# Kernel optimization log

Hardware: AMD Instinct MI355X
Metric: run time of the kernel (lower is better)

Reference implementation:

```python
import jax, jax.numpy as jnp
import numpy as np

B, C, H, W = 4, 64, 256, 256
HEADS = 8
WIN = 8            # window_size = (8, 8)
SPA_INNER = 64


def setup_inputs() -> dict:
    key = jax.random.key(0)
    ks = jax.random.split(key, 13)
    r = lambda k, s: jax.random.normal(k, s, dtype=jnp.float32)
    lin = lambda k, out_d, in_d: r(k, (out_d, in_d)) * (1.0 / np.sqrt(in_d))
    seq = WIN * WIN
    return {
        "x": r(ks[0], (B, C, H, W)),
        "pan_feature": r(ks[1], (B, C // 2, H, W)),
        "W_pan_q": lin(ks[2], SPA_INNER // 2, C // 2),
        "W_pan_k": lin(ks[3], SPA_INNER // 2, C // 2),
        "W_v1": lin(ks[4], SPA_INNER, C),
        "W_v2": lin(ks[5], SPA_INNER, C),
        "W_k2": lin(ks[6], SPA_INNER // 2, C),
        "W_q1c": lin(ks[7], SPA_INNER // 2, C),
        "W_k1c": lin(ks[8], SPA_INNER // 2, C),
        "W_inner_out": lin(ks[9], C, SPA_INNER),
        "W_inter_out": lin(ks[10], C, SPA_INNER),
        # trunc_normal_(std=1, a=-2, b=2) learned positional biases
        "pos_inner": jnp.clip(r(ks[11], (1, HEADS, seq, seq)), -2.0, 2.0),
        "pos_color": jnp.clip(r(ks[12], (1, HEADS, SPA_INNER // 2, SPA_INNER // 2)), -2.0, 2.0),
    }


def _mha(q, k, v, pos, heads, scale):
    # q,k,v: [B', n, h*d]  -> standard MHA with additive positional bias
    Bp, n, _ = q.shape
    sp = lambda t: t.reshape(Bp, n, heads, -1).transpose(0, 2, 1, 3)  # b h n d
    qh, kh, vh = sp(q) * scale, sp(k), sp(v)
    attn = jax.nn.softmax(jnp.einsum('bhid,bhjd->bhij', qh, kh) + pos, axis=-1)
    o = jnp.einsum('bhij,bhjd->bhid', attn, vh)
    return o.transpose(0, 2, 1, 3).reshape(Bp, n, -1)


def _mha_color(q, k, v, pos, heads, scale):
    # torch rearranges 'b (h d) n -> b h n d': dim1 (window area) is split
    # into heads, attention runs over the channel axis (dim2).
    Bp, hd, n = q.shape
    sp = lambda t: t.reshape(Bp, heads, hd // heads, n).transpose(0, 1, 3, 2)  # b h n d
    qh, kh, vh = sp(q) * scale, sp(k), sp(v)
    attn = jax.nn.softmax(jnp.einsum('bhid,bhjd->bhij', qh, kh) + pos, axis=-1)
    o = jnp.einsum('bhij,bhjd->bhid', attn, vh)
    return o.transpose(0, 1, 3, 2).reshape(Bp, hd, n)


def _inter_attn(q, k, v, heads):
    # elementwise cosine-similarity gating over the head-dim, no softmax
    Bp, n, dq = q.shape
    qh = q.reshape(Bp, n, heads, dq // heads).transpose(0, 2, 3, 1)  # b h d n
    kh = k.reshape(Bp, n, heads, dq // heads).transpose(0, 2, 3, 1)
    vh = v.reshape(Bp, n, heads, -1).transpose(0, 2, 1, 3)           # b h n d
    cos = jnp.sum(qh * kh, axis=2) / (jnp.linalg.norm(qh, axis=2) * jnp.linalg.norm(kh, axis=2))  # b h n
    o = cos[..., None] * vh
    return o.transpose(0, 2, 1, 3).reshape(Bp, n, -1)


def reference(x, pan_feature, W_pan_q, W_pan_k, W_v1, W_v2, W_k2, W_q1c, W_k1c,
              W_inner_out, W_inter_out, pos_inner, pos_color):
    b, c, h, w = x.shape
    hl = wl = WIN
    hn, wn = h // hl, w // wl

    def part(t):  # b c (hn hl) (wn wl) -> (b hn wn) (hl wl) c
        bb, cc = t.shape[0], t.shape[1]
        return t.reshape(bb, cc, hn, hl, wn, wl).transpose(0, 2, 4, 3, 5, 1).reshape(bb * hn * wn, hl * wl, cc)

    pan = part(pan_feature)       # [B', 64, c//2]
    xf = part(x)                  # [B', 64, c]

    pan_q = pan @ W_pan_q.T       # [B', 64, spa_inner//2]
    pan_k = pan @ W_pan_k.T
    x_v1 = xf @ W_v1.T            # [B', 64, spa_inner]
    half = x_v1.shape[-1] // 2
    v1_pan, v1_color = x_v1[..., :half], x_v1[..., half:]

    # inner spatial attention (scale uses inner_dim=spa_inner_dim, as in source)
    scale_inner = (SPA_INNER // HEADS) ** -0.5
    out_pan = _mha(pan_q, pan_k, v1_pan, pos_inner, HEADS, scale_inner)

    # inner color attention (scale uses inner_dim=window area)
    q1c = xf @ W_q1c.T
    k1c = xf @ W_k1c.T
    scale_color = ((hl * wl) // HEADS) ** -0.5
    out_color = _mha_color(q1c, k1c, v1_color, pos_color, HEADS, scale_color)

    out = jnp.concatenate([out_pan, out_color], axis=-1) @ W_inner_out.T  # [B', 64, c]
    x_v2 = out @ W_v2.T
    x_k2 = out @ W_k2.T
    out = _inter_attn(pan_q, x_k2, x_v2, HEADS)
    out = out @ W_inter_out.T     # [B', 64, c]

    cc = out.shape[-1]
    # (b hn wn) (hl wl) c -> b c (hn hl) (wn wl)
    out = out.reshape(b, hn, wn, hl, wl, cc).transpose(0, 5, 1, 3, 2, 4).reshape(b, cc, h, w)
    return out
```

## Files before the change

kernel.cpp:

```cpp
#include <hip/hip_runtime.h>


typedef __attribute__((ext_vector_type(8))) short short8;
typedef __attribute__((ext_vector_type(4))) float floatx4;

#define CCH  64
#define HH   256
#define WWD  256
#define HWsz (HH*WWD)
#define CHW  (CCH*HH*WWD)

#define OWPQ  0
#define OWPK  1024
#define OWV1  2048
#define OWV2  6144
#define OWK2  10240
#define OWQ1C 12288
#define OWK1C 14336
#define OWIO  16384
#define OWINT 20480
#define WTOT  24576

__device__ __forceinline__ unsigned int f2bf_u(float f) {
    unsigned int u = __builtin_bit_cast(unsigned int, f);
    u += 0x7FFFu + ((u >> 16) & 1u);
    return u >> 16;
}
__device__ __forceinline__ float bfu2f(unsigned int b) {
    return __builtin_bit_cast(float, b << 16);
}

template <int K, int N, int SA, int SO>
__device__ __forceinline__ void proj(const float* __restrict__ A,
                                     const unsigned short* __restrict__ Wh,
                                     const unsigned short* __restrict__ Wl,
                                     float* __restrict__ O,
                                     int wave, int lane) {
    constexpr int KS = K / 32;
    constexpr int NT = N / 16;
    const int l15 = lane & 15;
    const int quad = lane >> 4;
    const int m0 = wave * 16;

    union Frag { short8 v; unsigned int u[4]; };
    Frag ah[KS], al[KS];
#pragma unroll
    for (int kk = 0; kk < KS; ++kk) {
        const float4* ap = (const float4*)(A + (m0 + l15) * SA + kk * 32 + quad * 8);
        float4 fa = ap[0], fb = ap[1];
        float ff[8] = {fa.x, fa.y, fa.z, fa.w, fb.x, fb.y, fb.z, fb.w};
#pragma unroll
        for (int j2 = 0; j2 < 4; ++j2) {
            float f0 = ff[2 * j2], f1 = ff[2 * j2 + 1];
            unsigned int h0 = f2bf_u(f0), h1 = f2bf_u(f1);
            float r0 = f0 - bfu2f(h0), r1 = f1 - bfu2f(h1);
            ah[kk].u[j2] = h0 | (h1 << 16);
            al[kk].u[j2] = f2bf_u(r0) | (f2bf_u(r1) << 16);
        }
    }

#pragma unroll
    for (int nt = 0; nt < NT; ++nt) {
        floatx4 acc = {0.f, 0.f, 0.f, 0.f};
#pragma unroll
        for (int kk = 0; kk < KS; ++kk) {
            const int wo = (nt * 16 + l15) * K + kk * 32 + quad * 8;
            short8 bh = *(const short8*)(Wh + wo);
            short8 bl = *(const short8*)(Wl + wo);
            acc = __builtin_amdgcn_mfma_f32_16x16x32_bf16(ah[kk].v, bh, acc, 0, 0, 0);
            acc = __builtin_amdgcn_mfma_f32_16x16x32_bf16(al[kk].v, bh, acc, 0, 0, 0);
            acc = __builtin_amdgcn_mfma_f32_16x16x32_bf16(ah[kk].v, bl, acc, 0, 0, 0);
        }
#pragma unroll
        for (int r = 0; r < 4; ++r)
            O[(m0 + quad * 4 + r) * SO + nt * 16 + l15] = acc[r];
    }
}

__global__ void cvt_w(const float* __restrict__ w0, const float* __restrict__ w1,
                      const float* __restrict__ w2, const float* __restrict__ w3,
                      const float* __restrict__ w4, const float* __restrict__ w5,
                      const float* __restrict__ w6, const float* __restrict__ w7,
                      const float* __restrict__ w8, unsigned short* __restrict__ o) {
    int i = blockIdx.x * 256 + threadIdx.x;
    const float* src; int off;
    if      (i < 1024)  { src = w0; off = 0; }
    else if (i < 2048)  { src = w1; off = 1024; }
    else if (i < 6144)  { src = w2; off = 2048; }
    else if (i < 10240) { src = w3; off = 6144; }
    else if (i < 12288) { src = w4; off = 10240; }
    else if (i < 14336) { src = w5; off = 12288; }
    else if (i < 16384) { src = w6; off = 14336; }
    else if (i < 20480) { src = w7; off = 16384; }
    else                { src = w8; off = 20480; }
    float f = src[i - off];
    unsigned int h = f2bf_u(f);
    o[i] = (unsigned short)h;
    o[WTOT + i] = (unsigned short)f2bf_u(f - bfu2f(h));
}

__global__ __launch_bounds__(256, 2) void in2ma_main(
    const float* __restrict__ x, const float* __restrict__ pan,
    const float* __restrict__ posi, const float* __restrict__ posc,
    const unsigned short* __restrict__ wb, float* __restrict__ out) {
    __shared__ __align__(16) float s_xf[64 * 68];
    __shared__ __align__(16) float s_cat[64 * 68];
    __shared__ __align__(16) float s_v1[64 * 66];
    __shared__ __align__(16) float s_qk[64 * 66];
    __shared__ __align__(16) float s_k2[64 * 34];

    const int tid  = threadIdx.x;
    const int wave = tid >> 6;
    const int lane = tid & 63;
    const int wid  = blockIdx.x;
    const int b    = wid >> 10;
    const int hn_i = (wid >> 5) & 31;
    const int wn_i = wid & 31;
    const int h0 = hn_i * 8, w0 = wn_i * 8;

    const float scale = 0.35355339059327373f;
    const unsigned short* wlo = wb + WTOT;

    {
        const int c = tid >> 2, i = tid & 3;
        const float* xp = x + (size_t)b * CHW + (size_t)c * HWsz + (size_t)h0 * WWD + w0;
#pragma unroll
        for (int r = 0; r < 2; ++r) {
            const int hl = i * 2 + r;
            const float4* p = (const float4*)(xp + hl * WWD);
            float4 a = p[0], q = p[1];
            float* d = s_xf + (hl * 8) * 68 + c;
            d[0 * 68] = a.x; d[1 * 68] = a.y; d[2 * 68] = a.z; d[3 * 68] = a.w;
            d[4 * 68] = q.x; d[5 * 68] = q.y; d[6 * 68] = q.z; d[7 * 68] = q.w;
        }
        if (tid < 128) {
            const int c2 = tid >> 2, i2 = tid & 3;
            const float* pp = pan + (size_t)b * (CHW / 2) + (size_t)c2 * HWsz + (size_t)h0 * WWD + w0;
#pragma unroll
            for (int r = 0; r < 2; ++r) {
                const int hl = i2 * 2 + r;
                const float4* p = (const float4*)(pp + hl * WWD);
                float4 a = p[0], q = p[1];
                float* d = s_cat + (hl * 8) * 68 + c2;
                d[0 * 68] = a.x; d[1 * 68] = a.y; d[2 * 68] = a.z; d[3 * 68] = a.w;
                d[4 * 68] = q.x; d[5 * 68] = q.y; d[6 * 68] = q.z; d[7 * 68] = q.w;
            }
        }
    }
    __syncthreads();

    proj<32, 32, 68, 66>(s_cat,      wb + OWPQ,  wlo + OWPQ,  s_qk,      wave, lane);
    proj<32, 32, 68, 66>(s_cat,      wb + OWPK,  wlo + OWPK,  s_qk + 32, wave, lane);
    proj<64, 64, 68, 66>(s_xf,       wb + OWV1,  wlo + OWV1,  s_v1,      wave, lane);
    proj<64, 32, 68, 68>(s_xf,       wb + OWQ1C, wlo + OWQ1C, s_cat + 32, wave, lane);
    proj<64, 32, 68, 34>(s_xf,       wb + OWK1C, wlo + OWK1C, s_k2,      wave, lane);
    __syncthreads();

#pragma unroll
    for (int hh = 0; hh < 2; ++hh) {
        const int h = wave + hh * 4;
        const float* qp = s_qk + lane * 66 + 4 * h;
        float q0 = qp[0], q1 = qp[1], q2 = qp[2], q3 = qp[3];
        const float4* pp4 = (const float4*)(posi + h * 4096 + lane * 64);
        float lrow[64];
        float s = 0.f;
#pragma unroll
        for (int t4 = 0; t4 < 16; ++t4) {
            float4 pv = pp4[t4];
            float pvv[4] = {pv.x, pv.y, pv.z, pv.w};
#pragma unroll
            for (int u = 0; u < 4; ++u) {
                const int t = t4 * 4 + u;
                const float* kp = s_qk + t * 66 + 32 + 4 * h;
                float d = q0 * kp[0] + q1 * kp[1] + q2 * kp[2] + q3 * kp[3];
                float e = __expf(d * scale + pvv[u]);
                lrow[t] = e; s += e;
            }
        }
        const float inv = 1.f / s;
        float o0 = 0.f, o1 = 0.f, o2 = 0.f, o3 = 0.f;
#pragma unroll
        for (int t = 0; t < 64; ++t) {
            const float* vp = s_v1 + t * 66 + 4 * h;
            float p = lrow[t];
            o0 += p * vp[0]; o1 += p * vp[1]; o2 += p * vp[2]; o3 += p * vp[3];
        }
        float* op = s_cat + lane * 68 + 4 * h;
        op[0] = o0 * inv; op[1] = o1 * inv; op[2] = o2 * inv; op[3] = o3 * inv;
    }

    {
        const int h = wave * 2 + (lane >> 5);
        const int i = lane & 31;
        float q[8];
#pragma unroll
        for (int j = 0; j < 8; ++j) q[j] = s_cat[(8 * h + j) * 68 + 32 + i];
        float lr[32];
#pragma unroll
        for (int j = 0; j < 8; ++j) {
            const float* kp = s_k2 + (8 * h + j) * 34;
            const float qj = q[j];
#pragma unroll
            for (int t = 0; t < 32; ++t) {
                float kv = kp[t];
                if (j == 0) lr[t] = qj * kv; else lr[t] += qj * kv;
            }
        }
        const float4* pp4 = (const float4*)(posc + h * 1024 + i * 32);
        float s = 0.f;
#pragma unroll
        for (int t4 = 0; t4 < 8; ++t4) {
            float4 pv = pp4[t4];
            float pvv[4] = {pv.x, pv.y, pv.z, pv.w};
#pragma unroll
            for (int u = 0; u < 4; ++u) {
                const int t = t4 * 4 + u;
                float e = __expf(lr[t] * scale + pvv[u]);
                lr[t] = e; s += e;
            }
        }
        const float inv = 1.f / s;
#pragma unroll
        for (int j = 0; j < 8; ++j) {
            const float* vp = s_v1 + (8 * h + j) * 66 + 32;
            float acc = 0.f;
#pragma unroll
            for (int t = 0; t < 32; ++t) acc += lr[t] * vp[t];
            s_cat[(8 * h + j) * 68 + 32 + i] = acc * inv;
        }
    }
    __syncthreads();

    proj<64, 64, 68, 68>(s_cat, wb + OWIO, wlo + OWIO, s_xf, wave, lane);
    proj<64, 64, 68, 66>(s_xf,  wb + OWV2, wlo + OWV2, s_v1, wave, lane);
    proj<64, 32, 68, 34>(s_xf,  wb + OWK2, wlo + OWK2, s_k2, wave, lane);
    __syncthreads();

    {
        const int t = tid & 63;
        const int hb = tid >> 6;
#pragma unroll
        for (int r = 0; r < 2; ++r) {
            const int h = hb + r * 4;
            const float* qp = s_qk + t * 66 + 4 * h;
            const float* kp = s_k2 + t * 34 + 4 * h;
            float q0 = qp[0], q1 = qp[1], q2 = qp[2], q3 = qp[3];
            float k0 = kp[0], k1 = kp[1], k2 = kp[2], k3 = kp[3];
            float qq = q0 * q0 + q1 * q1 + q2 * q2 + q3 * q3;
            float kk = k0 * k0 + k1 * k1 + k2 * k2 + k3 * k3;
            float qk = q0 * k0 + q1 * k1 + q2 * k2 + q3 * k3;
            float cosv = qk * rsqrtf(qq * kk);
            const float* vp = s_v1 + t * 66 + 8 * h;
            float* op = s_cat + t * 68 + 8 * h;
#pragma unroll
            for (int j = 0; j < 8; ++j) op[j] = cosv * vp[j];
        }
    }
    __syncthreads();

    proj<64, 64, 68, 66>(s_cat, wb + OWINT, wlo + OWINT, s_v1, wave, lane);
    __syncthreads();

    {
        const int c = tid >> 2, i = tid & 3;
        float* op = out + (size_t)b * CHW + (size_t)c * HWsz + (size_t)h0 * WWD + w0;
#pragma unroll
        for (int r = 0; r < 2; ++r) {
            const int hl = i * 2 + r;
            float v[8];
#pragma unroll
            for (int wl = 0; wl < 8; ++wl)
                v[wl] = s_v1[(hl * 8 + wl) * 66 + c];
            float4* q = (float4*)(op + hl * WWD);
            float4 q0; q0.x = v[0]; q0.y = v[1]; q0.z = v[2]; q0.w = v[3];
            float4 q1; q1.x = v[4]; q1.y = v[5]; q1.z = v[6]; q1.w = v[7];
            q[0] = q0; q[1] = q1;
        }
    }
}

extern "C" void kernel_launch(void* const* d_in, const int* in_sizes, int n_in,
                              void* d_out, int out_size, void* d_ws, size_t ws_size,
                              hipStream_t stream) {
    (void)in_sizes; (void)n_in; (void)out_size; (void)ws_size;
    const float* x    = (const float*)d_in[0];
    const float* pan  = (const float*)d_in[1];
    const float* posi = (const float*)d_in[11];
    const float* posc = (const float*)d_in[12];
    unsigned short* wb = (unsigned short*)d_ws;

    cvt_w<<<WTOT / 256, 256, 0, stream>>>(
        (const float*)d_in[2], (const float*)d_in[3], (const float*)d_in[4],
        (const float*)d_in[5], (const float*)d_in[6], (const float*)d_in[7],
        (const float*)d_in[8], (const float*)d_in[9], (const float*)d_in[10], wb);

    in2ma_main<<<4096, 256, 0, stream>>>(x, pan, posi, posc, wb, (float*)d_out);
}
```

Measured before the change: 465.9 us.

## Use 512-thread blocks and split projections across eight waves

Doubles the workgroup to eight waves and redistributes the projection GEMMs and attention heads so each wave handles one head or one slice of a projection. Converted A fragments are reused across projections that read the same input, which cuts repeated fp32-to-split-bf16 conversion. Shared-memory row strides are padded to multiples of four so LDS accesses can use float4. The occupancy target is raised, which adds register pressure, and the inner-output projection is computed redundantly by paired waves.

```diff
diff --git a/kernel.cpp b/kernel.cpp
--- a/kernel.cpp
+++ b/kernel.cpp
@@ -30,22 +30,17 @@
     return __builtin_bit_cast(float, b << 16);
 }
 
-template <int K, int N, int SA, int SO>
-__device__ __forceinline__ void proj(const float* __restrict__ A,
-                                     const unsigned short* __restrict__ Wh,
-                                     const unsigned short* __restrict__ Wl,
-                                     float* __restrict__ O,
-                                     int wave, int lane) {
-    constexpr int KS = K / 32;
-    constexpr int NT = N / 16;
+union Frag { short8 v; unsigned int u[4]; };
+template <int KS> struct AF { Frag ah[KS], al[KS]; };
+
+template <int K, int SA>
+__device__ __forceinline__ AF<K / 32> load_afrag(const float* __restrict__ A,
+                                                 int m0, int lane) {
+    AF<K / 32> f;
     const int l15 = lane & 15;
     const int quad = lane >> 4;
-    const int m0 = wave * 16;
-
-    union Frag { short8 v; unsigned int u[4]; };
-    Frag ah[KS], al[KS];
-#pragma unroll
-    for (int kk = 0; kk < KS; ++kk) {
+#pragma unroll
+    for (int kk = 0; kk < K / 32; ++kk) {
         const float4* ap = (const float4*)(A + (m0 + l15) * SA + kk * 32 + quad * 8);
         float4 fa = ap[0], fb = ap[1];
         float ff[8] = {fa.x, fa.y, fa.z, fa.w, fb.x, fb.y, fb.z, fb.w};
@@ -54,26 +49,36 @@
             float f0 = ff[2 * j2], f1 = ff[2 * j2 + 1];
             unsigned int h0 = f2bf_u(f0), h1 = f2bf_u(f1);
             float r0 = f0 - bfu2f(h0), r1 = f1 - bfu2f(h1);
-            ah[kk].u[j2] = h0 | (h1 << 16);
-            al[kk].u[j2] = f2bf_u(r0) | (f2bf_u(r1) << 16);
-        }
-    }
-
+            f.ah[kk].u[j2] = h0 | (h1 << 16);
+            f.al[kk].u[j2] = f2bf_u(r0) | (f2bf_u(r1) << 16);
+        }
+    }
+    return f;
+}
+
+template <int K, int SO, int NT>
+__device__ __forceinline__ void mm(const AF<K / 32>& f,
+                                   const unsigned short* __restrict__ Wh,
+                                   const unsigned short* __restrict__ Wl,
+                                   float* __restrict__ O,
+                                   int m0, int n0, int lane) {
+    const int l15 = lane & 15;
+    const int quad = lane >> 4;
 #pragma unroll
     for (int nt = 0; nt < NT; ++nt) {
         floatx4 acc = {0.f, 0.f, 0.f, 0.f};
 #pragma unroll
-        for (int kk = 0; kk < KS; ++kk) {
-            const int wo = (nt * 16 + l15) * K + kk * 32 + quad * 8;
+        for (int kk = 0; kk < K / 32; ++kk) {
+            const int wo = (n0 + nt * 16 + l15) * K + kk * 32 + quad * 8;
             short8 bh = *(const short8*)(Wh + wo);
             short8 bl = *(const short8*)(Wl + wo);
-            acc = __builtin_amdgcn_mfma_f32_16x16x32_bf16(ah[kk].v, bh, acc, 0, 0, 0);
-            acc = __builtin_amdgcn_mfma_f32_16x16x32_bf16(al[kk].v, bh, acc, 0, 0, 0);
-            acc = __builtin_amdgcn_mfma_f32_16x16x32_bf16(ah[kk].v, bl, acc, 0, 0, 0);
+            acc = __builtin_amdgcn_mfma_f32_16x16x32_bf16(f.ah[kk].v, bh, acc, 0, 0, 0);
+            acc = __builtin_amdgcn_mfma_f32_16x16x32_bf16(f.al[kk].v, bh, acc, 0, 0, 0);
+            acc = __builtin_amdgcn_mfma_f32_16x16x32_bf16(f.ah[kk].v, bl, acc, 0, 0, 0);
         }
 #pragma unroll
         for (int r = 0; r < 4; ++r)
-            O[(m0 + quad * 4 + r) * SO + nt * 16 + l15] = acc[r];
+            O[(m0 + quad * 4 + r) * SO + n0 + nt * 16 + l15] = acc[r];
     }
 }
 
@@ -99,15 +104,15 @@
     o[WTOT + i] = (unsigned short)f2bf_u(f - bfu2f(h));
 }
 
-__global__ __launch_bounds__(256, 2) void in2ma_main(
+__global__ __launch_bounds__(512, 4) void in2ma_main(
     const float* __restrict__ x, const float* __restrict__ pan,
     const float* __restrict__ posi, const float* __restrict__ posc,
     const unsigned short* __restrict__ wb, float* __restrict__ out) {
     __shared__ __align__(16) float s_xf[64 * 68];
     __shared__ __align__(16) float s_cat[64 * 68];
-    __shared__ __align__(16) float s_v1[64 * 66];
-    __shared__ __align__(16) float s_qk[64 * 66];
-    __shared__ __align__(16) float s_k2[64 * 34];
+    __shared__ __align__(16) float s_v1[64 * 68];
+    __shared__ __align__(16) float s_qk[64 * 68];
+    __shared__ __align__(16) float s_k2[64 * 36];
 
     const int tid  = threadIdx.x;
     const int wave = tid >> 6;
@@ -122,48 +127,50 @@
     const unsigned short* wlo = wb + WTOT;
 
     {
-        const int c = tid >> 2, i = tid & 3;
-        const float* xp = x + (size_t)b * CHW + (size_t)c * HWsz + (size_t)h0 * WWD + w0;
-#pragma unroll
-        for (int r = 0; r < 2; ++r) {
-            const int hl = i * 2 + r;
-            const float4* p = (const float4*)(xp + hl * WWD);
-            float4 a = p[0], q = p[1];
-            float* d = s_xf + (hl * 8) * 68 + c;
-            d[0 * 68] = a.x; d[1 * 68] = a.y; d[2 * 68] = a.z; d[3 * 68] = a.w;
-            d[4 * 68] = q.x; d[5 * 68] = q.y; d[6 * 68] = q.z; d[7 * 68] = q.w;
-        }
-        if (tid < 128) {
-            const int c2 = tid >> 2, i2 = tid & 3;
-            const float* pp = pan + (size_t)b * (CHW / 2) + (size_t)c2 * HWsz + (size_t)h0 * WWD + w0;
-#pragma unroll
-            for (int r = 0; r < 2; ++r) {
-                const int hl = i2 * 2 + r;
-                const float4* p = (const float4*)(pp + hl * WWD);
-                float4 a = p[0], q = p[1];
-                float* d = s_cat + (hl * 8) * 68 + c2;
-                d[0 * 68] = a.x; d[1 * 68] = a.y; d[2 * 68] = a.z; d[3 * 68] = a.w;
-                d[4 * 68] = q.x; d[5 * 68] = q.y; d[6 * 68] = q.z; d[7 * 68] = q.w;
-            }
-        }
-    }
-    __syncthreads();
-
-    proj<32, 32, 68, 66>(s_cat,      wb + OWPQ,  wlo + OWPQ,  s_qk,      wave, lane);
-    proj<32, 32, 68, 66>(s_cat,      wb + OWPK,  wlo + OWPK,  s_qk + 32, wave, lane);
-    proj<64, 64, 68, 66>(s_xf,       wb + OWV1,  wlo + OWV1,  s_v1,      wave, lane);
-    proj<64, 32, 68, 68>(s_xf,       wb + OWQ1C, wlo + OWQ1C, s_cat + 32, wave, lane);
-    proj<64, 32, 68, 34>(s_xf,       wb + OWK1C, wlo + OWK1C, s_k2,      wave, lane);
-    __syncthreads();
-
-#pragma unroll
-    for (int hh = 0; hh < 2; ++hh) {
-        const int h = wave + hh * 4;
-        const float* qp = s_qk + lane * 66 + 4 * h;
-        float q0 = qp[0], q1 = qp[1], q2 = qp[2], q3 = qp[3];
+        const int c = lane, hl = wave;
+        const float* xp = x + (size_t)b * CHW + (size_t)c * HWsz
+                            + (size_t)(h0 + hl) * WWD + w0;
+        const float4* p = (const float4*)xp;
+        float4 a = p[0], q = p[1];
+        float* d = s_xf + (hl * 8) * 68 + c;
+        d[0 * 68] = a.x; d[1 * 68] = a.y; d[2 * 68] = a.z; d[3 * 68] = a.w;
+        d[4 * 68] = q.x; d[5 * 68] = q.y; d[6 * 68] = q.z; d[7 * 68] = q.w;
+        if (wave < 4) {
+            const int hl2 = wave * 2 + (lane >> 5);
+            const int c2 = lane & 31;
+            const float* pp = pan + (size_t)b * (CHW / 2) + (size_t)c2 * HWsz
+                                  + (size_t)(h0 + hl2) * WWD + w0;
+            const float4* p2 = (const float4*)pp;
+            float4 a2 = p2[0], q2 = p2[1];
+            float* d2 = s_cat + (hl2 * 8) * 68 + c2;
+            d2[0 * 68] = a2.x; d2[1 * 68] = a2.y; d2[2 * 68] = a2.z; d2[3 * 68] = a2.w;
+            d2[4 * 68] = q2.x; d2[5 * 68] = q2.y; d2[6 * 68] = q2.z; d2[7 * 68] = q2.w;
+        }
+    }
+    __syncthreads();
+
+    if (wave < 4) {
+        AF<2> f = load_afrag<64, 68>(s_xf, wave * 16, lane);
+        mm<64, 68, 4>(f, wb + OWV1, wlo + OWV1, s_v1, wave * 16, 0, lane);
+        AF<1> g = load_afrag<32, 68>(s_cat, wave * 16, lane);
+        mm<32, 68, 2>(g, wb + OWPQ, wlo + OWPQ, s_qk, wave * 16, 0, lane);
+    } else {
+        const int s = wave - 4;
+        AF<2> f = load_afrag<64, 68>(s_xf, s * 16, lane);
+        mm<64, 68, 2>(f, wb + OWQ1C, wlo + OWQ1C, s_cat + 32, s * 16, 0, lane);
+        mm<64, 36, 2>(f, wb + OWK1C, wlo + OWK1C, s_k2, s * 16, 0, lane);
+        AF<1> g = load_afrag<32, 68>(s_cat, s * 16, lane);
+        mm<32, 68, 2>(g, wb + OWPK, wlo + OWPK, s_qk + 32, s * 16, 0, lane);
+    }
+    __syncthreads();
+
+    {
+        const int h = wave;
+        const float4 qv = *(const float4*)(s_qk + lane * 68 + 4 * h);
+        const float q0 = qv.x, q1 = qv.y, q2 = qv.z, q3 = qv.w;
         const float4* pp4 = (const float4*)(posi + h * 4096 + lane * 64);
         float lrow[64];
-        float s = 0.f;
+        float sden = 0.f;
 #pragma unroll
         for (int t4 = 0; t4 < 16; ++t4) {
             float4 pv = pp4[t4];
@@ -171,25 +178,25 @@
 #pragma unroll
             for (int u = 0; u < 4; ++u) {
                 const int t = t4 * 4 + u;
-                const float* kp = s_qk + t * 66 + 32 + 4 * h;
-                float d = q0 * kp[0] + q1 * kp[1] + q2 * kp[2] + q3 * kp[3];
+                const float4 kv = *(const float4*)(s_qk + t * 68 + 32 + 4 * h);
+                float d = q0 * kv.x + q1 * kv.y + q2 * kv.z + q3 * kv.w;
                 float e = __expf(d * scale + pvv[u]);
-                lrow[t] = e; s += e;
+                lrow[t] = e; sden += e;
             }
         }
-        const float inv = 1.f / s;
+        const float inv = 1.f / sden;
         float o0 = 0.f, o1 = 0.f, o2 = 0.f, o3 = 0.f;
 #pragma unroll
         for (int t = 0; t < 64; ++t) {
-            const float* vp = s_v1 + t * 66 + 4 * h;
+            const float4 vv = *(const float4*)(s_v1 + t * 68 + 4 * h);
             float p = lrow[t];
-            o0 += p * vp[0]; o1 += p * vp[1]; o2 += p * vp[2]; o3 += p * vp[3];
-        }
-        float* op = s_cat + lane * 68 + 4 * h;
-        op[0] = o0 * inv; op[1] = o1 * inv; op[2] = o2 * inv; op[3] = o3 * inv;
-    }
-
-    {
+            o0 += p * vv.x; o1 += p * vv.y; o2 += p * vv.z; o3 += p * vv.w;
+        }
+        float4 ov; ov.x = o0 * inv; ov.y = o1 * inv; ov.z = o2 * inv; ov.w = o3 * inv;
+        *(float4*)(s_cat + lane * 68 + 4 * h) = ov;
+    }
+
+    if (wave < 4) {
         const int h = wave * 2 + (lane >> 5);
         const int i = lane & 31;
         float q[8];
@@ -198,7 +205,7 @@
         float lr[32];
 #pragma unroll
         for (int j = 0; j < 8; ++j) {
-            const float* kp = s_k2 + (8 * h + j) * 34;
+            const float* kp = s_k2 + (8 * h + j) * 36;
             const float qj = q[j];
 #pragma unroll
             for (int t = 0; t < 32; ++t) {
@@ -207,7 +214,7 @@
             }
         }
         const float4* pp4 = (const float4*)(posc + h * 1024 + i * 32);
-        float s = 0.f;
+        float sden = 0.f;
 #pragma unroll
         for (int t4 = 0; t4 < 8; ++t4) {
             float4 pv = pp4[t4];
@@ -216,13 +223,13 @@
             for (int u = 0; u < 4; ++u) {
                 const int t = t4 * 4 + u;
                 float e = __expf(lr[t] * scale + pvv[u]);
-                lr[t] = e; s += e;
+                lr[t] = e; sden += e;
             }
         }
-        const float inv = 1.f / s;
+        const float inv = 1.f / sden;
 #pragma unroll
         for (int j = 0; j < 8; ++j) {
-            const float* vp = s_v1 + (8 * h + j) * 66 + 32;
+            const float* vp = s_v1 + (8 * h + j) * 68 + 32;
             float acc = 0.f;
 #pragma unroll
             for (int t = 0; t < 32; ++t) acc += lr[t] * vp[t];
@@ -231,51 +238,55 @@
     }
     __syncthreads();
 
-    proj<64, 64, 68, 68>(s_cat, wb + OWIO, wlo + OWIO, s_xf, wave, lane);
-    proj<64, 64, 68, 66>(s_xf,  wb + OWV2, wlo + OWV2, s_v1, wave, lane);
-    proj<64, 32, 68, 34>(s_xf,  wb + OWK2, wlo + OWK2, s_k2, wave, lane);
-    __syncthreads();
-
-    {
-        const int t = tid & 63;
-        const int hb = tid >> 6;
-#pragma unroll
-        for (int r = 0; r < 2; ++r) {
-            const int h = hb + r * 4;
-            const float* qp = s_qk + t * 66 + 4 * h;
-            const float* kp = s_k2 + t * 34 + 4 * h;
-            float q0 = qp[0], q1 = qp[1], q2 = qp[2], q3 = qp[3];
-            float k0 = kp[0], k1 = kp[1], k2 = kp[2], k3 = kp[3];
-            float qq = q0 * q0 + q1 * q1 + q2 * q2 + q3 * q3;
-            float kk = k0 * k0 + k1 * k1 + k2 * k2 + k3 * k3;
-            float qk = q0 * k0 + q1 * k1 + q2 * k2 + q3 * k3;
-            float cosv = qk * rsqrtf(qq * kk);
-            const float* vp = s_v1 + t * 66 + 8 * h;
-            float* op = s_cat + t * 68 + 8 * h;
-#pragma unroll
-            for (int j = 0; j < 8; ++j) op[j] = cosv * vp[j];
-        }
-    }
-    __syncthreads();
-
-    proj<64, 64, 68, 66>(s_cat, wb + OWINT, wlo + OWINT, s_v1, wave, lane);
-    __syncthreads();
-
-    {
-        const int c = tid >> 2, i = tid & 3;
-        float* op = out + (size_t)b * CHW + (size_t)c * HWsz + (size_t)h0 * WWD + w0;
-#pragma unroll
-        for (int r = 0; r < 2; ++r) {
-            const int hl = i * 2 + r;
-            float v[8];
-#pragma unroll
-            for (int wl = 0; wl < 8; ++wl)
-                v[wl] = s_v1[(hl * 8 + wl) * 66 + c];
-            float4* q = (float4*)(op + hl * WWD);
-            float4 q0; q0.x = v[0]; q0.y = v[1]; q0.z = v[2]; q0.w = v[3];
-            float4 q1; q1.x = v[4]; q1.y = v[5]; q1.z = v[6]; q1.w = v[7];
-            q[0] = q0; q[1] = q1;
-        }
+    {
+        const int s = wave & 3;
+        AF<2> f = load_afrag<64, 68>(s_cat, s * 16, lane);
+        mm<64, 68, 4>(f, wb + OWIO, wlo + OWIO, s_xf, s * 16, 0, lane);
+        AF<2> g = load_afrag<64, 68>(s_xf, s * 16, lane);
+        if (wave < 4)
+            mm<64, 68, 4>(g, wb + OWV2, wlo + OWV2, s_v1, s * 16, 0, lane);
+        else
+            mm<64, 36, 2>(g, wb + OWK2, wlo + OWK2, s_k2, s * 16, 0, lane);
+    }
+    __syncthreads();
+
+    {
+        const int t = lane, h = wave;
+        const float4 qv = *(const float4*)(s_qk + t * 68 + 4 * h);
+        const float4 kv = *(const float4*)(s_k2 + t * 36 + 4 * h);
+        float qq = qv.x * qv.x + qv.y * qv.y + qv.z * qv.z + qv.w * qv.w;
+        float kk = kv.x * kv.x + kv.y * kv.y + kv.z * kv.z + kv.w * kv.w;
+        float qk = qv.x * kv.x + qv.y * kv.y + qv.z * kv.z + qv.w * kv.w;
+        float cosv = qk * rsqrtf(qq * kk);
+        const float4* vp = (const float4*)(s_v1 + t * 68 + 8 * h);
+        float4* op = (float4*)(s_cat + t * 68 + 8 * h);
+        float4 v0 = vp[0], v1 = vp[1];
+        float4 r0, r1;
+        r0.x = cosv * v0.x; r0.y = cosv * v0.y; r0.z = cosv * v0.z; r0.w = cosv * v0.w;
+        r1.x = cosv * v1.x; r1.y = cosv * v1.y; r1.z = cosv * v1.z; r1.w = cosv * v1.w;
+        op[0] = r0; op[1] = r1;
+    }
+    __syncthreads();
+
+    {
+        AF<2> f = load_afrag<64, 68>(s_cat, (wave >> 1) * 16, lane);
+        mm<64, 68, 2>(f, wb + OWINT, wlo + OWINT, s_v1,
+                      (wave >> 1) * 16, (wave & 1) * 32, lane);
+    }
+    __syncthreads();
+
+    {
+        const int c = lane, hl = wave;
+        float* op = out + (size_t)b * CHW + (size_t)c * HWsz
+                        + (size_t)(h0 + hl) * WWD + w0;
+        float v[8];
+#pragma unroll
+        for (int wl = 0; wl < 8; ++wl)
+            v[wl] = s_v1[(hl * 8 + wl) * 68 + c];
+        float4 q0; q0.x = v[0]; q0.y = v[1]; q0.z = v[2]; q0.w = v[3];
+        float4 q1; q1.x = v[4]; q1.y = v[5]; q1.z = v[6]; q1.w = v[7];
+        float4* q = (float4*)op;
+        q[0] = q0; q[1] = q1;
     }
 }
 
@@ -294,5 +305,5 @@
         (const float*)d_in[5], (const float*)d_in[6], (const float*)d_in[7],
         (const float*)d_in[8], (const float*)d_in[9], (const float*)d_in[10], wb);
 
-    in2ma_main<<<4096, 256, 0, stream>>>(x, pan, posi, posc, wb, (float*)d_out);
-}
+    in2ma_main<<<4096, 512, 0, stream>>>(x, pan, posi, posc, wb, (float*)d_out);
+}
```

Measured after the change: 692.2 us. 1.49x slower.
